# Performance work log

Hardware: AMD Instinct MI355X
Metric: run time of the kernel (lower is better)

## Reference

```python
import jax, jax.numpy as jnp
import numpy as np

B, S, H, D = 4, 8192, 8, 64  # batch, seq, heads, head_dim
M = 64                        # num random features
EPS = 1e-6


def setup_inputs() -> dict:
    key = jax.random.key(0)
    k1, k2, k3, k4 = jax.random.split(key, 4)
    qs = jax.random.normal(k1, (B, S, H, D), dtype=jnp.float32)
    ks = jax.random.normal(k2, (B, S, H, D), dtype=jnp.float32)
    vs = jax.random.normal(k3, (B, S, H, D), dtype=jnp.float32)
    proj = jax.random.normal(k4, (M, D), dtype=jnp.float32)
    return {"qs": qs, "ks": ks, "vs": vs, "proj": proj}


def _phi(x, proj):
    # stable positive softmax kernel: exp(x @ proj^T - ||x||^2/2) / sqrt(m)
    m = proj.shape[0]
    x_proj = jnp.einsum('...d,md->...m', x, proj)
    h = jnp.sum(jnp.square(x), axis=-1, keepdims=True) * 0.5
    return jnp.exp(x_proj - h) / jnp.sqrt(jnp.asarray(m, x.dtype))


def reference(qs, ks, vs, proj):
    Bq, Q, Hh, Dqk = qs.shape
    K = ks.shape[1]
    Dv = vs.shape[-1]
    # (B, S, H, D) -> (B*H, S, D)
    q = qs.transpose(0, 2, 1, 3).reshape(-1, Q, Dqk)
    k = ks.transpose(0, 2, 1, 3).reshape(-1, K, Dqk)
    v = vs.transpose(0, 2, 1, 3).reshape(-1, K, Dv)
    normalizer = 1.0 / jnp.power(jnp.asarray(Dqk, q.dtype), 0.25)
    q_prime = _phi(q * normalizer, proj)  # (B*H, Q, M)
    k_prime = _phi(k * normalizer, proj)  # (B*H, K, M)
    # fast_attend: linear-time attention
    c = jnp.concatenate([v, jnp.ones((*v.shape[:-1], 1), v.dtype)], axis=-1)  # (B*H, K, Dv+1)
    buf1 = jnp.einsum('bkm,bkc->bmc', k_prime, c)   # (B*H, M, Dv+1)
    buf2 = jnp.einsum('bqm,bmc->bqc', q_prime, buf1)  # (B*H, Q, Dv+1)
    num, den = buf2[..., :-1], buf2[..., -1]
    den = jnp.where(den < EPS, EPS, den)
    ctx = num / den[..., None]
    return ctx.reshape(Bq, Hh, Q, Dv).transpose(0, 2, 1, 3)
```

## Files before the change

### kernel.cpp

```cpp
#include <hip/hip_runtime.h>
#include <hip/hip_bf16.h>

#define S_ 8192
#define H_ 8
#define D_ 64
#define M_ 64
#define BH_ 32
#define CPK_ 80
#define NCH_ 16
#define ITERS_ 4
#define NCHQ 16
#define TILE 64
#define QTILES (S_ / NCHQ / TILE)

typedef short bf16x8 __attribute__((ext_vector_type(8)));
typedef float f32x4 __attribute__((ext_vector_type(4)));

constexpr float XS_ = 0.35355339059327373f * 1.4426950408889634f;
constexpr float HS_ = 0.34657359027997264f;
constexpr float EPS_ = 1e-6f;

__device__ __forceinline__ unsigned short f2bf(float f) {
    unsigned int u = __float_as_uint(f);
    u += 0x7FFFu + ((u >> 16) & 1u);
    return (unsigned short)(u >> 16);
}
__device__ __forceinline__ unsigned int pkbf(float lo, float hi) {
    __hip_bfloat162 t = __float22bfloat162_rn(float2{lo, hi});
    return *reinterpret_cast<unsigned int*>(&t);
}
__device__ __forceinline__ float fexp2(float x) { return __builtin_amdgcn_exp2f(x); }

#define MFMA(a, b, c) __builtin_amdgcn_mfma_f32_16x16x32_bf16((a), (b), (c), 0, 0, 0)
#define SWZ(byteoff, row) ((byteoff) ^ (((row) & 7) << 4))

__global__ void __launch_bounds__(256, 2)
fa_k(const float* __restrict__ ks, const float* __restrict__ vs,
     const float* __restrict__ proj, float* __restrict__ partial)
{
    const int chunk = blockIdx.x;
    const int bh    = blockIdx.y;
    const int b = bh >> 3, h = bh & 7;
    const int tid = threadIdx.x, wid = tid >> 6, lane = tid & 63;
    const int l15 = lane & 15, g = lane >> 4;

    __shared__ __align__(16) char vW[4][2][64 * 64];
    __shared__ float red[M_ * CPK_];

    const size_t rs = (size_t)H_ * D_;
    const float* kb = ks + ((size_t)b * S_ * H_ + h) * D_;
    const float* vb = vs + ((size_t)b * S_ * H_ + h) * D_;
    const int rbase = chunk * (ITERS_ * 128) + wid * 32;

    bf16x8 pf[4][2];
#pragma unroll
    for (int mt = 0; mt < 4; ++mt)
#pragma unroll
        for (int kk = 0; kk < 2; ++kk) {
            const float* p = proj + (mt * 16 + l15) * D_ + kk * 32 + g * 8;
            float4 a = *(const float4*)p, c = *(const float4*)(p + 4);
            union { bf16x8 v; unsigned int u[4]; } F;
            F.u[0] = pkbf(a.x, a.y); F.u[1] = pkbf(a.z, a.w);
            F.u[2] = pkbf(c.x, c.y); F.u[3] = pkbf(c.z, c.w);
            pf[mt][kk] = F.v;
        }

    bf16x8 onef = {0, 0, 0, 0, 0, 0, 0, 0};
    if (l15 == 0) {
#pragma unroll
        for (int j = 0; j < 8; ++j) onef[j] = (short)0x3F80;
    }

    f32x4 acc[4][5];
#pragma unroll
    for (int mt = 0; mt < 4; ++mt)
#pragma unroll
        for (int ci = 0; ci < 5; ++ci) acc[mt][ci] = (f32x4){0.f, 0.f, 0.f, 0.f};

    auto loadX = [&](const float* xb, int t, float4* xp) {
        const float* r0 = xb + (size_t)(rbase + t * 128 + l15) * rs;
        xp[0] = *(const float4*)(r0 + g * 8);
        xp[1] = *(const float4*)(r0 + g * 8 + 4);
        xp[2] = *(const float4*)(r0 + 32 + g * 8);
        xp[3] = *(const float4*)(r0 + 32 + g * 8 + 4);
        const float* r1 = r0 + 16 * rs;
        xp[4] = *(const float4*)(r1 + g * 8);
        xp[5] = *(const float4*)(r1 + g * 8 + 4);
        xp[6] = *(const float4*)(r1 + 32 + g * 8);
        xp[7] = *(const float4*)(r1 + 32 + g * 8 + 4);
    };

    auto storeV = [&](const float4* vp, int buf) {
        char* base = (char*)vW + wid * 8192 + buf * 4096;
        int id0 = ((l15 >> 2) & 3) * 8 + (l15 & 3);
#pragma unroll
        for (int s = 0; s < 2; ++s) {
            int id = id0 + 4 * s;
            float vv[16];
#pragma unroll
            for (int i = 0; i < 4; ++i) {
                float4 q = vp[4 * s + i];
                vv[4 * i + 0] = q.x; vv[4 * i + 1] = q.y;
                vv[4 * i + 2] = q.z; vv[4 * i + 3] = q.w;
            }
#pragma unroll
            for (int p2 = 0; p2 < 4; ++p2) {
                int cA = g * 8 + 2 * p2;
                unsigned int pA = pkbf(vv[2 * p2], vv[2 * p2 + 1]);
                *(unsigned short*)(base + cA * 64 + ((2 * id) ^ ((cA & 3) << 4))) =
                    (unsigned short)pA;
                int cB = cA + 1;
                *(unsigned short*)(base + cB * 64 + ((2 * id) ^ ((cB & 3) << 4))) =
                    (unsigned short)(pA >> 16);
                int cC = 32 + cA;
                unsigned int pB = pkbf(vv[8 + 2 * p2], vv[9 + 2 * p2]);
                *(unsigned short*)(base + cC * 64 + ((2 * id) ^ ((cC & 3) << 4))) =
                    (unsigned short)pB;
                int cD = cC + 1;
                *(unsigned short*)(base + cD * 64 + ((2 * id) ^ ((cD & 3) << 4))) =
                    (unsigned short)(pB >> 16);
            }
        }
    };

    auto body = [&](int t, const float4* kc, float4* kn, float4* vn) {
        if (t + 1 < ITERS_) { loadX(kb, t + 1, kn); loadX(vb, t + 1, vn); }

        float kx0[16], kx1[16];
#pragma unroll
        for (int i = 0; i < 4; ++i) {
            kx0[4*i+0] = kc[i].x * XS_; kx0[4*i+1] = kc[i].y * XS_;
            kx0[4*i+2] = kc[i].z * XS_; kx0[4*i+3] = kc[i].w * XS_;
            kx1[4*i+0] = kc[4+i].x * XS_; kx1[4*i+1] = kc[4+i].y * XS_;
            kx1[4*i+2] = kc[4+i].z * XS_; kx1[4*i+3] = kc[4+i].w * XS_;
        }
        float sq0 = 0.f, sq1 = 0.f;
#pragma unroll
        for (int j = 0; j < 16; ++j) { sq0 += kx0[j]*kx0[j]; sq1 += kx1[j]*kx1[j]; }
        sq0 += __shfl_xor(sq0, 16); sq0 += __shfl_xor(sq0, 32);
        sq1 += __shfl_xor(sq1, 16); sq1 += __shfl_xor(sq1, 32);
        float h0 = sq0 * HS_ + 3.0f, h1 = sq1 * HS_ + 3.0f;

        union { bf16x8 v; unsigned int u[4]; } A00, A01, A10, A11;
#pragma unroll
        for (int i = 0; i < 4; ++i) {
            A00.u[i] = pkbf(kx0[2*i], kx0[2*i+1]);
            A01.u[i] = pkbf(kx0[8+2*i], kx0[9+2*i]);
            A10.u[i] = pkbf(kx1[2*i], kx1[2*i+1]);
            A11.u[i] = pkbf(kx1[8+2*i], kx1[9+2*i]);
        }

        f32x4 pa0[4], pa1[4];
#pragma unroll
        for (int mt = 0; mt < 4; ++mt) {
            pa0[mt] = (f32x4){0.f, 0.f, 0.f, 0.f};
            pa0[mt] = MFMA(A00.v, pf[mt][0], pa0[mt]);
            pa0[mt] = MFMA(A01.v, pf[mt][1], pa0[mt]);
            pa1[mt] = (f32x4){0.f, 0.f, 0.f, 0.f};
            pa1[mt] = MFMA(A10.v, pf[mt][0], pa1[mt]);
            pa1[mt] = MFMA(A11.v, pf[mt][1], pa1[mt]);
        }

        float hr0[4], hr1[4];
#pragma unroll
        for (int r = 0; r < 4; ++r) {
            hr0[r] = __shfl(h0, 4 * g + r);
            hr1[r] = __shfl(h1, 4 * g + r);
        }

        bf16x8 eA[4];
#pragma unroll
        for (int mt = 0; mt < 4; ++mt) {
            union { bf16x8 v; unsigned int u[4]; } E;
            E.u[0] = pkbf(fexp2(pa0[mt][0]-hr0[0]), fexp2(pa0[mt][1]-hr0[1]));
            E.u[1] = pkbf(fexp2(pa0[mt][2]-hr0[2]), fexp2(pa0[mt][3]-hr0[3]));
            E.u[2] = pkbf(fexp2(pa1[mt][0]-hr1[0]), fexp2(pa1[mt][1]-hr1[1]));
            E.u[3] = pkbf(fexp2(pa1[mt][2]-hr1[2]), fexp2(pa1[mt][3]-hr1[3]));
            eA[mt] = E.v;
        }

        const char* rb2 = (const char*)vW + wid * 8192 + (t & 1) * 4096;
        bf16x8 vB[4];
#pragma unroll
        for (int ct = 0; ct < 4; ++ct) {
            int c = ct * 16 + l15;
            vB[ct] = *(const bf16x8*)(rb2 + c * 64 + ((16 * g) ^ ((c & 3) << 4)));
        }
#pragma unroll
        for (int mt = 0; mt < 4; ++mt) {
#pragma unroll
            for (int ct = 0; ct < 4; ++ct)
                acc[mt][ct] = MFMA(eA[mt], vB[ct], acc[mt][ct]);
            acc[mt][4] = MFMA(eA[mt], onef, acc[mt][4]);
        }

        if (t + 1 < ITERS_) storeV(vn, (t + 1) & 1);
    };

    float4 k0[8], k1[8], v0[8], v1[8];
    loadX(kb, 0, k0);
    loadX(vb, 0, v0);
    storeV(v0, 0);
    body(0, k0, k1, v1);
    body(1, k1, k0, v0);
    body(2, k0, k1, v1);
    body(3, k1, k0, v0);

    for (int i = tid; i < M_ * CPK_; i += 256) red[i] = 0.f;
    __syncthreads();
    for (int w = 0; w < 4; ++w) {
        if (wid == w) {
#pragma unroll
            for (int mt = 0; mt < 4; ++mt)
#pragma unroll
                for (int ct = 0; ct < 5; ++ct)
#pragma unroll
                    for (int r = 0; r < 4; ++r)
                        red[(mt*16 + 4*g + r) * CPK_ + ct*16 + l15] += acc[mt][ct][r];
        }
        __syncthreads();
    }
    float* dst = partial + ((size_t)bh * NCH_ + chunk) * (M_ * CPK_);
    for (int i = tid; i < M_ * CPK_; i += 256) dst[i] = red[i];
}

__global__ void __launch_bounds__(256)
fa_r(const float* __restrict__ partial, float* __restrict__ buf1, int nch)
{
    int e = blockIdx.x * 256 + threadIdx.x;
    if (e >= BH_ * M_ * CPK_) return;
    int bh = e / (M_ * CPK_);
    int r  = e - bh * (M_ * CPK_);
    const float* src = partial + (size_t)bh * nch * (M_ * CPK_) + r;
    float s0 = 0.f, s1 = 0.f, s2 = 0.f, s3 = 0.f;
    int ch = 0;
    for (; ch + 4 <= nch; ch += 4) {
        s0 += src[(size_t)(ch + 0) * (M_ * CPK_)];
        s1 += src[(size_t)(ch + 1) * (M_ * CPK_)];
        s2 += src[(size_t)(ch + 2) * (M_ * CPK_)];
        s3 += src[(size_t)(ch + 3) * (M_ * CPK_)];
    }
    for (; ch < nch; ++ch) s0 += src[(size_t)ch * (M_ * CPK_)];
    buf1[e] = (s0 + s1) + (s2 + s3);
}

__global__ void __launch_bounds__(256)
fa_q(const float* __restrict__ qs, const float* __restrict__ proj,
     const float* __restrict__ buf1, float* __restrict__ out)
{
    const int chunk = blockIdx.x;
    const int bh    = blockIdx.y;
    const int b = bh >> 3, h = bh & 7;
    const int tid = threadIdx.x, wid = tid >> 6, lane = tid & 63;
    const int l15 = lane & 15, g = lane >> 4;

    __shared__ __align__(16) char eLb[2][TILE * M_ * 2];
    __shared__ __align__(16) char b1tb[CPK_ * M_ * 2];

    const int rows = S_ / NCHQ;
    const int s0 = chunk * rows;
    const size_t rs = (size_t)H_ * D_;
    const float* qb = qs + ((size_t)b * S_ * H_ + h) * D_;

    const float* b1 = buf1 + (size_t)bh * (M_ * CPK_);
    for (int i = tid; i < M_ * CPK_; i += 256) {
        int m = i / CPK_, c = i - m * CPK_;
        *(unsigned short*)(b1tb + SWZ(c * 128 + 2 * m, c)) = f2bf(b1[i]);
    }

    bf16x8 pf[4][2];
#pragma unroll
    for (int mt = 0; mt < 4; ++mt)
#pragma unroll
        for (int kk = 0; kk < 2; ++kk) {
            const float* p = proj + (mt * 16 + l15) * D_ + kk * 32 + g * 8;
            float4 a = *(const float4*)p, c = *(const float4*)(p + 4);
            union { bf16x8 v; unsigned int u[4]; } F;
            F.u[0] = pkbf(a.x, a.y); F.u[1] = pkbf(a.z, a.w);
            F.u[2] = pkbf(c.x, c.y); F.u[3] = pkbf(c.z, c.w);
            pf[mt][kk] = F.v;
        }
    __syncthreads();

    bf16x8 af3[5][2];
#pragma unroll
    for (int ci = 0; ci < 5; ++ci)
#pragma unroll
        for (int kk = 0; kk < 2; ++kk) {
            int c = ci * 16 + l15;
            af3[ci][kk] = *(const bf16x8*)(b1tb + SWZ(c * 128 + 16 * g + 64 * kk, c));
        }

    auto loadQ = [&](int t, float4* qp) {
        int sb = s0 + t * TILE;
        const float* qrow = qb + (size_t)(sb + wid * 16 + l15) * rs;
        qp[0] = *(const float4*)(qrow + g * 8);
        qp[1] = *(const float4*)(qrow + g * 8 + 4);
        qp[2] = *(const float4*)(qrow + 32 + g * 8);
        qp[3] = *(const float4*)(qrow + 32 + g * 8 + 4);
    };

    auto body = [&](int t, int p, const float4* qc, float4* qn) {
        if (t + 1 < QTILES) loadQ(t + 1, qn);

        float kx[16];
#pragma unroll
        for (int i = 0; i < 4; ++i) {
            kx[4 * i + 0] = qc[i].x * XS_; kx[4 * i + 1] = qc[i].y * XS_;
            kx[4 * i + 2] = qc[i].z * XS_; kx[4 * i + 3] = qc[i].w * XS_;
        }
        float sq = 0.f;
#pragma unroll
        for (int j = 0; j < 16; ++j) sq += kx[j] * kx[j];
        sq += __shfl_xor(sq, 16);
        sq += __shfl_xor(sq, 32);
        float hrow = sq * HS_ + 3.0f;

        union { bf16x8 v; unsigned int u[4]; } A0, A1;
#pragma unroll
        for (int i = 0; i < 4; ++i) {
            A0.u[i] = pkbf(kx[2 * i], kx[2 * i + 1]);
            A1.u[i] = pkbf(kx[8 + 2 * i], kx[9 + 2 * i]);
        }

        f32x4 pa[4];
#pragma unroll
        for (int mt = 0; mt < 4; ++mt) {
            pa[mt] = (f32x4){0.f, 0.f, 0.f, 0.f};
            pa[mt] = MFMA(A0.v, pf[mt][0], pa[mt]);
            pa[mt] = MFMA(A1.v, pf[mt][1], pa[mt]);
        }

        float hr[4];
#pragma unroll
        for (int r = 0; r < 4; ++r) hr[r] = __shfl(hrow, 4 * g + r);

        char* elp = eLb[p];
#pragma unroll
        for (int mt = 0; mt < 4; ++mt) {
            int m = mt * 16 + l15;
            float e0 = fexp2(pa[mt][0] - hr[0]);
            float e1 = fexp2(pa[mt][1] - hr[1]);
            float e2 = fexp2(pa[mt][2] - hr[2]);
            float e3 = fexp2(pa[mt][3] - hr[3]);
            unsigned int p01 = pkbf(e0, e1), p23 = pkbf(e2, e3);
            int q0 = wid * 16 + 4 * g;
            *(unsigned short*)(elp + SWZ((q0 + 0) * 128 + 2 * m, q0 + 0)) =
                (unsigned short)p01;
            *(unsigned short*)(elp + SWZ((q0 + 1) * 128 + 2 * m, q0 + 1)) =
                (unsigned short)(p01 >> 16);
            *(unsigned short*)(elp + SWZ((q0 + 2) * 128 + 2 * m, q0 + 2)) =
                (unsigned short)p23;
            *(unsigned short*)(elp + SWZ((q0 + 3) * 128 + 2 * m, q0 + 3)) =
                (unsigned short)(p23 >> 16);
        }
        __syncthreads();

        bf16x8 b3[2];
        {
            int qrow = wid * 16 + l15;
            b3[0] = *(const bf16x8*)(elp + SWZ(qrow * 128 + 16 * g, qrow));
            b3[1] = *(const bf16x8*)(elp + SWZ(qrow * 128 + 16 * g + 64, qrow));
        }
        f32x4 dt[5];
#pragma unroll
        for (int ci = 0; ci < 5; ++ci) {
            dt[ci] = (f32x4){0.f, 0.f, 0.f, 0.f};
            dt[ci] = MFMA(af3[ci][0], b3[0], dt[ci]);
            dt[ci] = MFMA(af3[ci][1], b3[1], dt[ci]);
        }

        float den = __shfl(dt[4][0], l15);
        float rd = 1.0f / fmaxf(den, EPS_);

        int sg = s0 + t * TILE + wid * 16 + l15;
        size_t base = (((size_t)b * S_ + sg) * H_ + h) * D_;
#pragma unroll
        for (int ci = 0; ci < 4; ++ci) {
            f32x4 o;
#pragma unroll
            for (int r = 0; r < 4; ++r) o[r] = dt[ci][r] * rd;
            *(f32x4*)(out + base + ci * 16 + 4 * g) = o;
        }
    };

    float4 qa[4], qb2[4];
    loadQ(0, qa);
    for (int t = 0; t < QTILES; t += 2) {
        body(t, 0, qa, qb2);
        body(t + 1, 1, qb2, qa);
    }
}

extern "C" void kernel_launch(void* const* d_in, const int* in_sizes, int n_in,
                              void* d_out, int out_size, void* d_ws, size_t ws_size,
                              hipStream_t stream)
{
    const float* qs   = (const float*)d_in[0];
    const float* ks   = (const float*)d_in[1];
    const float* vs   = (const float*)d_in[2];
    const float* proj = (const float*)d_in[3];
    float* out = (float*)d_out;

    float* partial = (float*)d_ws;
    float* buf1 = partial + (size_t)BH_ * NCH_ * (M_ * CPK_);

    fa_k<<<dim3(NCH_, BH_), 256, 0, stream>>>(ks, vs, proj, partial);
    int nred = (BH_ * M_ * CPK_ + 255) / 256;
    fa_r<<<dim3(nred), 256, 0, stream>>>(partial, buf1, NCH_);
    fa_q<<<dim3(NCHQ, BH_), 256, 0, stream>>>(qs, proj, buf1, out);
}
```

Measured before the change: 74.45 us.

## Restructure K/V feature kernel to load all heads contiguously per batch

The K/V reduction kernel now assigns one block per (sequence chunk, batch) with 8 waves, one per head. Each tile reads 16 full sequence rows, covering all heads, as contiguous float4 loads, and stages bf16 K and transposed V plus the row norms through shared memory. The old design used strided per-head row loads with one block per (chunk, head). Each wave now writes its partial accumulator straight to global memory, dropping the shared-memory cross-wave reduction, and the chunk count rises to 64 or 32 depending on workspace size. The exp step is deferred to pair two 16-row tiles per MFMA, which adds block-wide barriers per tile and doubles the partial buffer the reduction kernel must read.

```diff
diff --git a/kernel.cpp b/kernel.cpp
--- a/kernel.cpp
+++ b/kernel.cpp
@@ -7,8 +7,6 @@
 #define M_ 64
 #define BH_ 32
 #define CPK_ 80
-#define NCH_ 16
-#define ITERS_ 4
 #define NCHQ 16
 #define TILE 64
 #define QTILES (S_ / NCHQ / TILE)
@@ -34,23 +32,23 @@
 #define MFMA(a, b, c) __builtin_amdgcn_mfma_f32_16x16x32_bf16((a), (b), (c), 0, 0, 0)
 #define SWZ(byteoff, row) ((byteoff) ^ (((row) & 7) << 4))
 
-__global__ void __launch_bounds__(256, 2)
+__global__ void __launch_bounds__(512, 2)
 fa_k(const float* __restrict__ ks, const float* __restrict__ vs,
-     const float* __restrict__ proj, float* __restrict__ partial)
+     const float* __restrict__ proj, float* __restrict__ partial,
+     int sch, int tiles)
 {
     const int chunk = blockIdx.x;
-    const int bh    = blockIdx.y;
-    const int b = bh >> 3, h = bh & 7;
-    const int tid = threadIdx.x, wid = tid >> 6, lane = tid & 63;
+    const int b     = blockIdx.y;
+    const int tid = threadIdx.x, w8 = tid >> 6, lane = tid & 63;
     const int l15 = lane & 15, g = lane >> 4;
 
-    __shared__ __align__(16) char vW[4][2][64 * 64];
-    __shared__ float red[M_ * CPK_];
-
-    const size_t rs = (size_t)H_ * D_;
-    const float* kb = ks + ((size_t)b * S_ * H_ + h) * D_;
-    const float* vb = vs + ((size_t)b * S_ * H_ + h) * D_;
-    const int rbase = chunk * (ITERS_ * 128) + wid * 32;
+    __shared__ __align__(16) char kT[16 * 8 * 128];
+    __shared__ __align__(16) char vT[8 * 64 * 64];
+    __shared__ float hL[16 * 8];
+
+    const int s0 = chunk * tiles * 16;
+    const float4* kf4 = (const float4*)(ks + ((size_t)b * S_ + s0) * (H_ * D_));
+    const float4* vf4 = (const float4*)(vs + ((size_t)b * S_ + s0) * (H_ * D_));
 
     bf16x8 pf[4][2];
 #pragma unroll
@@ -77,151 +75,120 @@
 #pragma unroll
         for (int ci = 0; ci < 5; ++ci) acc[mt][ci] = (f32x4){0.f, 0.f, 0.f, 0.f};
 
-    auto loadX = [&](const float* xb, int t, float4* xp) {
-        const float* r0 = xb + (size_t)(rbase + t * 128 + l15) * rs;
-        xp[0] = *(const float4*)(r0 + g * 8);
-        xp[1] = *(const float4*)(r0 + g * 8 + 4);
-        xp[2] = *(const float4*)(r0 + 32 + g * 8);
-        xp[3] = *(const float4*)(r0 + 32 + g * 8 + 4);
-        const float* r1 = r0 + 16 * rs;
-        xp[4] = *(const float4*)(r1 + g * 8);
-        xp[5] = *(const float4*)(r1 + g * 8 + 4);
-        xp[6] = *(const float4*)(r1 + 32 + g * 8);
-        xp[7] = *(const float4*)(r1 + 32 + g * 8 + 4);
-    };
-
-    auto storeV = [&](const float4* vp, int buf) {
-        char* base = (char*)vW + wid * 8192 + buf * 4096;
-        int id0 = ((l15 >> 2) & 3) * 8 + (l15 & 3);
-#pragma unroll
-        for (int s = 0; s < 2; ++s) {
-            int id = id0 + 4 * s;
-            float vv[16];
-#pragma unroll
-            for (int i = 0; i < 4; ++i) {
-                float4 q = vp[4 * s + i];
-                vv[4 * i + 0] = q.x; vv[4 * i + 1] = q.y;
-                vv[4 * i + 2] = q.z; vv[4 * i + 3] = q.w;
+    f32x4 paE[4];
+    float hrE[4];
+
+    auto loadT = [&](int t, float4* kp, float4* vp) {
+        size_t base = (size_t)t * 2048 + w8 * 256 + lane;
+#pragma unroll
+        for (int j = 0; j < 4; ++j) {
+            kp[j] = kf4[base + j * 64];
+            vp[j] = vf4[base + j * 64];
+        }
+    };
+
+    auto stage = [&](const float4* kp, const float4* vp, int tpar) {
+#pragma unroll
+        for (int j = 0; j < 4; ++j) {
+            int vrow = w8 * 16 + j * 4 + g;
+            int sl = vrow >> 3, h = vrow & 7;
+            float4 kx = kp[j];
+            kx.x *= XS_; kx.y *= XS_; kx.z *= XS_; kx.w *= XS_;
+            float sq = kx.x*kx.x + kx.y*kx.y + kx.z*kx.z + kx.w*kx.w;
+            sq += __shfl_xor(sq, 1); sq += __shfl_xor(sq, 2);
+            sq += __shfl_xor(sq, 4); sq += __shfl_xor(sq, 8);
+            if (l15 == 0) hL[sl * 8 + h] = sq * HS_ + 3.0f;
+
+            unsigned long long kpk = (unsigned long long)pkbf(kx.x, kx.y)
+                                   | ((unsigned long long)pkbf(kx.z, kx.w) << 32);
+            int kb2 = (sl * 1024 + h * 128 + l15 * 8) ^ (((sl + h) & 7) << 4);
+            *(unsigned long long*)(kT + kb2) = kpk;
+
+            unsigned int v01 = pkbf(vp[j].x, vp[j].y);
+            unsigned int v23 = pkbf(vp[j].z, vp[j].w);
+            int row32 = tpar * 16 + sl;
+            int slot2 = 2 * (((row32 >> 2) & 3) * 8 + 4 * (row32 >> 4) + (row32 & 3));
+            char* vbase = vT + h * 4096 + l15 * 256;
+            *(unsigned short*)(vbase +   0 + (slot2 ^  0)) = (unsigned short)v01;
+            *(unsigned short*)(vbase +  64 + (slot2 ^ 16)) = (unsigned short)(v01 >> 16);
+            *(unsigned short*)(vbase + 128 + (slot2 ^ 32)) = (unsigned short)v23;
+            *(unsigned short*)(vbase + 192 + (slot2 ^ 48)) = (unsigned short)(v23 >> 16);
+        }
+    };
+
+    auto consume = [&](int t) {
+        float hrow = hL[l15 * 8 + w8];
+        int key = ((l15 + w8) & 7) << 4;
+        int kb2 = l15 * 1024 + w8 * 128 + g * 16;
+        bf16x8 kA0 = *(const bf16x8*)(kT + (kb2 ^ key));
+        bf16x8 kA1 = *(const bf16x8*)(kT + ((kb2 + 64) ^ key));
+        f32x4 pa[4];
+#pragma unroll
+        for (int mt = 0; mt < 4; ++mt) {
+            pa[mt] = (f32x4){0.f, 0.f, 0.f, 0.f};
+            pa[mt] = MFMA(kA0, pf[mt][0], pa[mt]);
+            pa[mt] = MFMA(kA1, pf[mt][1], pa[mt]);
+        }
+        float hr[4];
+#pragma unroll
+        for (int r = 0; r < 4; ++r) hr[r] = __shfl(hrow, 4 * g + r);
+
+        if ((t & 1) == 0) {
+#pragma unroll
+            for (int mt = 0; mt < 4; ++mt) paE[mt] = pa[mt];
+#pragma unroll
+            for (int r = 0; r < 4; ++r) hrE[r] = hr[r];
+        } else {
+            bf16x8 eA[4];
+#pragma unroll
+            for (int mt = 0; mt < 4; ++mt) {
+                union { bf16x8 v; unsigned int u[4]; } E;
+                E.u[0] = pkbf(fexp2(paE[mt][0]-hrE[0]), fexp2(paE[mt][1]-hrE[1]));
+                E.u[1] = pkbf(fexp2(paE[mt][2]-hrE[2]), fexp2(paE[mt][3]-hrE[3]));
+                E.u[2] = pkbf(fexp2(pa[mt][0]-hr[0]),   fexp2(pa[mt][1]-hr[1]));
+                E.u[3] = pkbf(fexp2(pa[mt][2]-hr[2]),   fexp2(pa[mt][3]-hr[3]));
+                eA[mt] = E.v;
             }
-#pragma unroll
-            for (int p2 = 0; p2 < 4; ++p2) {
-                int cA = g * 8 + 2 * p2;
-                unsigned int pA = pkbf(vv[2 * p2], vv[2 * p2 + 1]);
-                *(unsigned short*)(base + cA * 64 + ((2 * id) ^ ((cA & 3) << 4))) =
-                    (unsigned short)pA;
-                int cB = cA + 1;
-                *(unsigned short*)(base + cB * 64 + ((2 * id) ^ ((cB & 3) << 4))) =
-                    (unsigned short)(pA >> 16);
-                int cC = 32 + cA;
-                unsigned int pB = pkbf(vv[8 + 2 * p2], vv[9 + 2 * p2]);
-                *(unsigned short*)(base + cC * 64 + ((2 * id) ^ ((cC & 3) << 4))) =
-                    (unsigned short)pB;
-                int cD = cC + 1;
-                *(unsigned short*)(base + cD * 64 + ((2 * id) ^ ((cD & 3) << 4))) =
-                    (unsigned short)(pB >> 16);
+            const char* vb2 = vT + w8 * 4096;
+            bf16x8 vB[4];
+#pragma unroll
+            for (int ct = 0; ct < 4; ++ct) {
+                int c = ct * 16 + l15;
+                vB[ct] = *(const bf16x8*)(vb2 + c * 64 + ((16 * g) ^ ((c & 3) << 4)));
             }
-        }
-    };
-
-    auto body = [&](int t, const float4* kc, float4* kn, float4* vn) {
-        if (t + 1 < ITERS_) { loadX(kb, t + 1, kn); loadX(vb, t + 1, vn); }
-
-        float kx0[16], kx1[16];
-#pragma unroll
-        for (int i = 0; i < 4; ++i) {
-            kx0[4*i+0] = kc[i].x * XS_; kx0[4*i+1] = kc[i].y * XS_;
-            kx0[4*i+2] = kc[i].z * XS_; kx0[4*i+3] = kc[i].w * XS_;
-            kx1[4*i+0] = kc[4+i].x * XS_; kx1[4*i+1] = kc[4+i].y * XS_;
-            kx1[4*i+2] = kc[4+i].z * XS_; kx1[4*i+3] = kc[4+i].w * XS_;
-        }
-        float sq0 = 0.f, sq1 = 0.f;
-#pragma unroll
-        for (int j = 0; j < 16; ++j) { sq0 += kx0[j]*kx0[j]; sq1 += kx1[j]*kx1[j]; }
-        sq0 += __shfl_xor(sq0, 16); sq0 += __shfl_xor(sq0, 32);
-        sq1 += __shfl_xor(sq1, 16); sq1 += __shfl_xor(sq1, 32);
-        float h0 = sq0 * HS_ + 3.0f, h1 = sq1 * HS_ + 3.0f;
-
-        union { bf16x8 v; unsigned int u[4]; } A00, A01, A10, A11;
-#pragma unroll
-        for (int i = 0; i < 4; ++i) {
-            A00.u[i] = pkbf(kx0[2*i], kx0[2*i+1]);
-            A01.u[i] = pkbf(kx0[8+2*i], kx0[9+2*i]);
-            A10.u[i] = pkbf(kx1[2*i], kx1[2*i+1]);
-            A11.u[i] = pkbf(kx1[8+2*i], kx1[9+2*i]);
-        }
-
-        f32x4 pa0[4], pa1[4];
-#pragma unroll
-        for (int mt = 0; mt < 4; ++mt) {
-            pa0[mt] = (f32x4){0.f, 0.f, 0.f, 0.f};
-            pa0[mt] = MFMA(A00.v, pf[mt][0], pa0[mt]);
-            pa0[mt] = MFMA(A01.v, pf[mt][1], pa0[mt]);
-            pa1[mt] = (f32x4){0.f, 0.f, 0.f, 0.f};
-            pa1[mt] = MFMA(A10.v, pf[mt][0], pa1[mt]);
-            pa1[mt] = MFMA(A11.v, pf[mt][1], pa1[mt]);
-        }
-
-        float hr0[4], hr1[4];
-#pragma unroll
-        for (int r = 0; r < 4; ++r) {
-            hr0[r] = __shfl(h0, 4 * g + r);
-            hr1[r] = __shfl(h1, 4 * g + r);
-        }
-
-        bf16x8 eA[4];
-#pragma unroll
-        for (int mt = 0; mt < 4; ++mt) {
-            union { bf16x8 v; unsigned int u[4]; } E;
-            E.u[0] = pkbf(fexp2(pa0[mt][0]-hr0[0]), fexp2(pa0[mt][1]-hr0[1]));
-            E.u[1] = pkbf(fexp2(pa0[mt][2]-hr0[2]), fexp2(pa0[mt][3]-hr0[3]));
-            E.u[2] = pkbf(fexp2(pa1[mt][0]-hr1[0]), fexp2(pa1[mt][1]-hr1[1]));
-            E.u[3] = pkbf(fexp2(pa1[mt][2]-hr1[2]), fexp2(pa1[mt][3]-hr1[3]));
-            eA[mt] = E.v;
-        }
-
-        const char* rb2 = (const char*)vW + wid * 8192 + (t & 1) * 4096;
-        bf16x8 vB[4];
-#pragma unroll
-        for (int ct = 0; ct < 4; ++ct) {
-            int c = ct * 16 + l15;
-            vB[ct] = *(const bf16x8*)(rb2 + c * 64 + ((16 * g) ^ ((c & 3) << 4)));
-        }
-#pragma unroll
-        for (int mt = 0; mt < 4; ++mt) {
-#pragma unroll
-            for (int ct = 0; ct < 4; ++ct)
-                acc[mt][ct] = MFMA(eA[mt], vB[ct], acc[mt][ct]);
-            acc[mt][4] = MFMA(eA[mt], onef, acc[mt][4]);
-        }
-
-        if (t + 1 < ITERS_) storeV(vn, (t + 1) & 1);
-    };
-
-    float4 k0[8], k1[8], v0[8], v1[8];
-    loadX(kb, 0, k0);
-    loadX(vb, 0, v0);
-    storeV(v0, 0);
-    body(0, k0, k1, v1);
-    body(1, k1, k0, v0);
-    body(2, k0, k1, v1);
-    body(3, k1, k0, v0);
-
-    for (int i = tid; i < M_ * CPK_; i += 256) red[i] = 0.f;
-    __syncthreads();
-    for (int w = 0; w < 4; ++w) {
-        if (wid == w) {
-#pragma unroll
-            for (int mt = 0; mt < 4; ++mt)
-#pragma unroll
-                for (int ct = 0; ct < 5; ++ct)
-#pragma unroll
-                    for (int r = 0; r < 4; ++r)
-                        red[(mt*16 + 4*g + r) * CPK_ + ct*16 + l15] += acc[mt][ct][r];
-        }
-        __syncthreads();
-    }
-    float* dst = partial + ((size_t)bh * NCH_ + chunk) * (M_ * CPK_);
-    for (int i = tid; i < M_ * CPK_; i += 256) dst[i] = red[i];
+#pragma unroll
+            for (int mt = 0; mt < 4; ++mt) {
+#pragma unroll
+                for (int ct = 0; ct < 4; ++ct)
+                    acc[mt][ct] = MFMA(eA[mt], vB[ct], acc[mt][ct]);
+                acc[mt][4] = MFMA(eA[mt], onef, acc[mt][4]);
+            }
+        }
+    };
+
+    float4 kA_[4], vA_[4], kB_[4], vB_[4];
+    loadT(0, kA_, vA_);
+    for (int t = 0; t < tiles; t += 2) {
+        __syncthreads();
+        stage(kA_, vA_, 0);
+        if (t + 1 < tiles) loadT(t + 1, kB_, vB_);
+        __syncthreads();
+        consume(t);
+        __syncthreads();
+        stage(kB_, vB_, 1);
+        if (t + 2 < tiles) loadT(t + 2, kA_, vA_);
+        __syncthreads();
+        consume(t + 1);
+    }
+
+    float* dst = partial + ((size_t)(b * 8 + w8) * sch + chunk) * (M_ * CPK_);
+#pragma unroll
+    for (int mt = 0; mt < 4; ++mt)
+#pragma unroll
+        for (int ct = 0; ct < 5; ++ct)
+#pragma unroll
+            for (int r = 0; r < 4; ++r)
+                dst[(mt * 16 + 4 * g + r) * CPK_ + ct * 16 + l15] = acc[mt][ct][r];
 }
 
 __global__ void __launch_bounds__(256)
@@ -402,11 +369,16 @@
     const float* proj = (const float*)d_in[3];
     float* out = (float*)d_out;
 
+    size_t per = (size_t)(M_ * CPK_) * sizeof(float);
+    int sch = 64;
+    if ((size_t)BH_ * (size_t)(sch + 1) * per > ws_size) sch = 32;
+    int tiles = S_ / sch / 16;
+
     float* partial = (float*)d_ws;
-    float* buf1 = partial + (size_t)BH_ * NCH_ * (M_ * CPK_);
-
-    fa_k<<<dim3(NCH_, BH_), 256, 0, stream>>>(ks, vs, proj, partial);
+    float* buf1 = partial + (size_t)BH_ * sch * (M_ * CPK_);
+
+    fa_k<<<dim3(sch, 4), 512, 0, stream>>>(ks, vs, proj, partial, sch, tiles);
     int nred = (BH_ * M_ * CPK_ + 255) / 256;
-    fa_r<<<dim3(nred), 256, 0, stream>>>(partial, buf1, NCH_);
+    fa_r<<<dim3(nred), 256, 0, stream>>>(partial, buf1, sch);
     fa_q<<<dim3(NCHQ, BH_), 256, 0, stream>>>(qs, proj, buf1, out);
 }
```

Result: slower. 111.6 us (+49.9%).

## Restructure K/V feature kernel into 16-row steps with two-deep prefetch

Applied to the files above, without the earlier changes.

Each wave now owns a contiguous 128-row span and walks it in eight 16-row steps instead of four 32-row steps. Loads are issued two steps ahead through a three-buffer rotation, and the projection results of even steps are held until the odd step, so the exp and accumulation MFMAs still run on 32-row pairs. The aim is smaller register footprint per step and deeper memory prefetch to hide global-load latency. It adds more, smaller loads and LDS writes per step, and the stores to a V buffer slot are not separated by any barrier from reads of that slot.

```diff
diff --git a/kernel.cpp b/kernel.cpp
--- a/kernel.cpp
+++ b/kernel.cpp
@@ -8,7 +8,6 @@
 #define BH_ 32
 #define CPK_ 80
 #define NCH_ 16
-#define ITERS_ 4
 #define NCHQ 16
 #define TILE 64
 #define QTILES (S_ / NCHQ / TILE)
@@ -44,13 +43,13 @@
     const int tid = threadIdx.x, wid = tid >> 6, lane = tid & 63;
     const int l15 = lane & 15, g = lane >> 4;
 
-    __shared__ __align__(16) char vW[4][2][64 * 64];
+    __shared__ __align__(16) char vT[4][2][64 * 64];
     __shared__ float red[M_ * CPK_];
 
     const size_t rs = (size_t)H_ * D_;
     const float* kb = ks + ((size_t)b * S_ * H_ + h) * D_;
     const float* vb = vs + ((size_t)b * S_ * H_ + h) * D_;
-    const int rbase = chunk * (ITERS_ * 128) + wid * 32;
+    const int rbase = chunk * 512 + wid * 128;
 
     bf16x8 pf[4][2];
 #pragma unroll
@@ -77,134 +76,130 @@
 #pragma unroll
         for (int ci = 0; ci < 5; ++ci) acc[mt][ci] = (f32x4){0.f, 0.f, 0.f, 0.f};
 
-    auto loadX = [&](const float* xb, int t, float4* xp) {
-        const float* r0 = xb + (size_t)(rbase + t * 128 + l15) * rs;
-        xp[0] = *(const float4*)(r0 + g * 8);
-        xp[1] = *(const float4*)(r0 + g * 8 + 4);
-        xp[2] = *(const float4*)(r0 + 32 + g * 8);
-        xp[3] = *(const float4*)(r0 + 32 + g * 8 + 4);
-        const float* r1 = r0 + 16 * rs;
-        xp[4] = *(const float4*)(r1 + g * 8);
-        xp[5] = *(const float4*)(r1 + g * 8 + 4);
-        xp[6] = *(const float4*)(r1 + 32 + g * 8);
-        xp[7] = *(const float4*)(r1 + 32 + g * 8 + 4);
+    f32x4 paE[4];
+    float hrE[4];
+
+    auto loadX = [&](int t, float4* kp, float4* vp) {
+        const float* kr = kb + (size_t)(rbase + t * 16 + l15) * rs;
+        kp[0] = *(const float4*)(kr + g * 8);
+        kp[1] = *(const float4*)(kr + g * 8 + 4);
+        kp[2] = *(const float4*)(kr + 32 + g * 8);
+        kp[3] = *(const float4*)(kr + 32 + g * 8 + 4);
+        const float* vr = vb + (size_t)(rbase + t * 16 + l15) * rs;
+        vp[0] = *(const float4*)(vr + g * 8);
+        vp[1] = *(const float4*)(vr + g * 8 + 4);
+        vp[2] = *(const float4*)(vr + 32 + g * 8);
+        vp[3] = *(const float4*)(vr + 32 + g * 8 + 4);
     };
 
-    auto storeV = [&](const float4* vp, int buf) {
-        char* base = (char*)vW + wid * 8192 + buf * 4096;
-        int id0 = ((l15 >> 2) & 3) * 8 + (l15 & 3);
-#pragma unroll
-        for (int s = 0; s < 2; ++s) {
-            int id = id0 + 4 * s;
+    auto body = [&](int t, const float4* kc, const float4* vc,
+                    float4* kn2, float4* vn2) {
+        if (t + 2 < 8) loadX(t + 2, kn2, vn2);
+
+        float kx[16];
+#pragma unroll
+        for (int i = 0; i < 4; ++i) {
+            kx[4*i+0] = kc[i].x * XS_; kx[4*i+1] = kc[i].y * XS_;
+            kx[4*i+2] = kc[i].z * XS_; kx[4*i+3] = kc[i].w * XS_;
+        }
+        float sq = 0.f;
+#pragma unroll
+        for (int j = 0; j < 16; ++j) sq += kx[j] * kx[j];
+        sq += __shfl_xor(sq, 16);
+        sq += __shfl_xor(sq, 32);
+        float hrow = sq * HS_ + 3.0f;
+
+        union { bf16x8 v; unsigned int u[4]; } A0, A1;
+#pragma unroll
+        for (int i = 0; i < 4; ++i) {
+            A0.u[i] = pkbf(kx[2*i], kx[2*i+1]);
+            A1.u[i] = pkbf(kx[8+2*i], kx[9+2*i]);
+        }
+
+        f32x4 pa[4];
+#pragma unroll
+        for (int mt = 0; mt < 4; ++mt) {
+            pa[mt] = (f32x4){0.f, 0.f, 0.f, 0.f};
+            pa[mt] = MFMA(A0.v, pf[mt][0], pa[mt]);
+            pa[mt] = MFMA(A1.v, pf[mt][1], pa[mt]);
+        }
+
+        float hr[4];
+#pragma unroll
+        for (int r = 0; r < 4; ++r) hr[r] = __shfl(hrow, 4 * g + r);
+
+        {
+            char* vtp = (char*)vT + wid * 8192 + ((t >> 1) & 1) * 4096;
+            int slot2 = 2 * (((l15 >> 2) & 3) * 8 + 4 * (t & 1) + (l15 & 3));
             float vv[16];
 #pragma unroll
             for (int i = 0; i < 4; ++i) {
-                float4 q = vp[4 * s + i];
-                vv[4 * i + 0] = q.x; vv[4 * i + 1] = q.y;
-                vv[4 * i + 2] = q.z; vv[4 * i + 3] = q.w;
+                vv[4*i+0] = vc[i].x; vv[4*i+1] = vc[i].y;
+                vv[4*i+2] = vc[i].z; vv[4*i+3] = vc[i].w;
             }
 #pragma unroll
             for (int p2 = 0; p2 < 4; ++p2) {
                 int cA = g * 8 + 2 * p2;
-                unsigned int pA = pkbf(vv[2 * p2], vv[2 * p2 + 1]);
-                *(unsigned short*)(base + cA * 64 + ((2 * id) ^ ((cA & 3) << 4))) =
+                unsigned int pA = pkbf(vv[2*p2], vv[2*p2+1]);
+                *(unsigned short*)(vtp + cA * 64 + (slot2 ^ ((cA & 3) << 4))) =
                     (unsigned short)pA;
                 int cB = cA + 1;
-                *(unsigned short*)(base + cB * 64 + ((2 * id) ^ ((cB & 3) << 4))) =
+                *(unsigned short*)(vtp + cB * 64 + (slot2 ^ ((cB & 3) << 4))) =
                     (unsigned short)(pA >> 16);
                 int cC = 32 + cA;
-                unsigned int pB = pkbf(vv[8 + 2 * p2], vv[9 + 2 * p2]);
-                *(unsigned short*)(base + cC * 64 + ((2 * id) ^ ((cC & 3) << 4))) =
+                unsigned int pB = pkbf(vv[8+2*p2], vv[9+2*p2]);
+                *(unsigned short*)(vtp + cC * 64 + (slot2 ^ ((cC & 3) << 4))) =
                     (unsigned short)pB;
                 int cD = cC + 1;
-                *(unsigned short*)(base + cD * 64 + ((2 * id) ^ ((cD & 3) << 4))) =
+                *(unsigned short*)(vtp + cD * 64 + (slot2 ^ ((cD & 3) << 4))) =
                     (unsigned short)(pB >> 16);
             }
         }
+
+        if ((t & 1) == 0) {
+#pragma unroll
+            for (int mt = 0; mt < 4; ++mt) paE[mt] = pa[mt];
+#pragma unroll
+            for (int r = 0; r < 4; ++r) hrE[r] = hr[r];
+        } else {
+            bf16x8 eA[4];
+#pragma unroll
+            for (int mt = 0; mt < 4; ++mt) {
+                union { bf16x8 v; unsigned int u[4]; } E;
+                E.u[0] = pkbf(fexp2(paE[mt][0]-hrE[0]), fexp2(paE[mt][1]-hrE[1]));
+                E.u[1] = pkbf(fexp2(paE[mt][2]-hrE[2]), fexp2(paE[mt][3]-hrE[3]));
+                E.u[2] = pkbf(fexp2(pa[mt][0]-hr[0]),   fexp2(pa[mt][1]-hr[1]));
+                E.u[3] = pkbf(fexp2(pa[mt][2]-hr[2]),   fexp2(pa[mt][3]-hr[3]));
+                eA[mt] = E.v;
+            }
+            const char* vb2 = (const char*)vT + wid * 8192 + ((t >> 1) & 1) * 4096;
+            bf16x8 vB[4];
+#pragma unroll
+            for (int ct = 0; ct < 4; ++ct) {
+                int c = ct * 16 + l15;
+                vB[ct] = *(const bf16x8*)(vb2 + c * 64 + ((16 * g) ^ ((c & 3) << 4)));
+            }
+#pragma unroll
+            for (int mt = 0; mt < 4; ++mt) {
+#pragma unroll
+                for (int ct = 0; ct < 4; ++ct)
+                    acc[mt][ct] = MFMA(eA[mt], vB[ct], acc[mt][ct]);
+                acc[mt][4] = MFMA(eA[mt], onef, acc[mt][4]);
+            }
+        }
     };
 
-    auto body = [&](int t, const float4* kc, float4* kn, float4* vn) {
-        if (t + 1 < ITERS_) { loadX(kb, t + 1, kn); loadX(vb, t + 1, vn); }
-
-        float kx0[16], kx1[16];
-#pragma unroll
-        for (int i = 0; i < 4; ++i) {
-            kx0[4*i+0] = kc[i].x * XS_; kx0[4*i+1] = kc[i].y * XS_;
-            kx0[4*i+2] = kc[i].z * XS_; kx0[4*i+3] = kc[i].w * XS_;
-            kx1[4*i+0] = kc[4+i].x * XS_; kx1[4*i+1] = kc[4+i].y * XS_;
-            kx1[4*i+2] = kc[4+i].z * XS_; kx1[4*i+3] = kc[4+i].w * XS_;
-        }
-        float sq0 = 0.f, sq1 = 0.f;
-#pragma unroll
-        for (int j = 0; j < 16; ++j) { sq0 += kx0[j]*kx0[j]; sq1 += kx1[j]*kx1[j]; }
-        sq0 += __shfl_xor(sq0, 16); sq0 += __shfl_xor(sq0, 32);
-        sq1 += __shfl_xor(sq1, 16); sq1 += __shfl_xor(sq1, 32);
-        float h0 = sq0 * HS_ + 3.0f, h1 = sq1 * HS_ + 3.0f;
-
-        union { bf16x8 v; unsigned int u[4]; } A00, A01, A10, A11;
-#pragma unroll
-        for (int i = 0; i < 4; ++i) {
-            A00.u[i] = pkbf(kx0[2*i], kx0[2*i+1]);
-            A01.u[i] = pkbf(kx0[8+2*i], kx0[9+2*i]);
-            A10.u[i] = pkbf(kx1[2*i], kx1[2*i+1]);
-            A11.u[i] = pkbf(kx1[8+2*i], kx1[9+2*i]);
-        }
-
-        f32x4 pa0[4], pa1[4];
-#pragma unroll
-        for (int mt = 0; mt < 4; ++mt) {
-            pa0[mt] = (f32x4){0.f, 0.f, 0.f, 0.f};
-            pa0[mt] = MFMA(A00.v, pf[mt][0], pa0[mt]);
-            pa0[mt] = MFMA(A01.v, pf[mt][1], pa0[mt]);
-            pa1[mt] = (f32x4){0.f, 0.f, 0.f, 0.f};
-            pa1[mt] = MFMA(A10.v, pf[mt][0], pa1[mt]);
-            pa1[mt] = MFMA(A11.v, pf[mt][1], pa1[mt]);
-        }
-
-        float hr0[4], hr1[4];
-#pragma unroll
-        for (int r = 0; r < 4; ++r) {
-            hr0[r] = __shfl(h0, 4 * g + r);
-            hr1[r] = __shfl(h1, 4 * g + r);
-        }
-
-        bf16x8 eA[4];
-#pragma unroll
-        for (int mt = 0; mt < 4; ++mt) {
-            union { bf16x8 v; unsigned int u[4]; } E;
-            E.u[0] = pkbf(fexp2(pa0[mt][0]-hr0[0]), fexp2(pa0[mt][1]-hr0[1]));
-            E.u[1] = pkbf(fexp2(pa0[mt][2]-hr0[2]), fexp2(pa0[mt][3]-hr0[3]));
-            E.u[2] = pkbf(fexp2(pa1[mt][0]-hr1[0]), fexp2(pa1[mt][1]-hr1[1]));
-            E.u[3] = pkbf(fexp2(pa1[mt][2]-hr1[2]), fexp2(pa1[mt][3]-hr1[3]));
-            eA[mt] = E.v;
-        }
-
-        const char* rb2 = (const char*)vW + wid * 8192 + (t & 1) * 4096;
-        bf16x8 vB[4];
-#pragma unroll
-        for (int ct = 0; ct < 4; ++ct) {
-            int c = ct * 16 + l15;
-            vB[ct] = *(const bf16x8*)(rb2 + c * 64 + ((16 * g) ^ ((c & 3) << 4)));
-        }
-#pragma unroll
-        for (int mt = 0; mt < 4; ++mt) {
-#pragma unroll
-            for (int ct = 0; ct < 4; ++ct)
-                acc[mt][ct] = MFMA(eA[mt], vB[ct], acc[mt][ct]);
-            acc[mt][4] = MFMA(eA[mt], onef, acc[mt][4]);
-        }
-
-        if (t + 1 < ITERS_) storeV(vn, (t + 1) & 1);
-    };
-
-    float4 k0[8], k1[8], v0[8], v1[8];
-    loadX(kb, 0, k0);
-    loadX(vb, 0, v0);
-    storeV(v0, 0);
-    body(0, k0, k1, v1);
-    body(1, k1, k0, v0);
-    body(2, k0, k1, v1);
-    body(3, k1, k0, v0);
+    float4 kA[4], vA[4], kB[4], vB_[4], kC[4], vC[4];
+    loadX(0, kA, vA);
+    loadX(1, kB, vB_);
+    body(0, kA, vA, kC, vC);
+    body(1, kB, vB_, kA, vA);
+    body(2, kC, vC, kB, vB_);
+    body(3, kA, vA, kC, vC);
+    body(4, kB, vB_, kA, vA);
+    body(5, kC, vC, kB, vB_);
+    body(6, kA, vA, kC, vC);
+    body(7, kB, vB_, kA, vA);
 
     for (int i = tid; i < M_ * CPK_; i += 256) red[i] = 0.f;
     __syncthreads();
```

New measurement: 74.15 us. Within noise of the previous version (-0.4%).
